# Optimization experiments

Hardware: AMD Instinct MI355X
Metric: run time of the kernel (lower is better)

The kernel has to match this reference:

```python
import jax, jax.numpy as jnp
import numpy as np

N = 100000      # nodes
E = 1600000     # edges (before self loops)
G = 64          # graphs (drones)
H = 4           # heads
C = 64          # hidden_channels (per-head dim, concat=False)
NODE_F = 32
DRONE_F = 16
OUT = 32
L = 2           # num_layers
LN_EPS = 1e-5
NEG_SLOPE = 0.2


def setup_inputs() -> dict:
    key = jax.random.key(0)
    ks = jax.random.split(key, 20)
    gn = lambda k, shape, s=0.1: jax.random.normal(k, shape, jnp.float32) * s
    inp = {}
    inp["x"] = jax.random.normal(ks[0], (N, NODE_F), jnp.float32)
    inp["drone_feat"] = jax.random.normal(ks[1], (G, DRONE_F), jnp.float32)
    inp["edge_index"] = jax.random.randint(ks[2], (2, E), 0, N, jnp.int32)
    inp["batch"] = jnp.sort(jax.random.randint(ks[3], (N,), 0, G, jnp.int32))
    inp["node_W"] = gn(ks[4], (C, NODE_F)); inp["node_b"] = jnp.zeros((C,), jnp.float32)
    inp["drone_W"] = gn(ks[5], (C, DRONE_F)); inp["drone_b"] = jnp.zeros((C,), jnp.float32)
    for l in range(L):
        kk = jax.random.split(ks[6 + l], 3)
        inp[f"convW{l}"] = gn(kk[0], (H * C, C))
        inp[f"att_src{l}"] = gn(kk[1], (H, C))
        inp[f"att_dst{l}"] = gn(kk[2], (H, C))
        inp[f"convb{l}"] = jnp.zeros((C,), jnp.float32)
        inp[f"ln_g{l}"] = jnp.ones((C,), jnp.float32)
        inp[f"ln_b{l}"] = jnp.zeros((C,), jnp.float32)
    inp["out_W"] = gn(ks[10], (OUT, C)); inp["out_b"] = jnp.zeros((OUT,), jnp.float32)
    return inp


def _layer_norm(x, g, b):
    mu = jnp.mean(x, axis=-1, keepdims=True)
    var = jnp.mean((x - mu) ** 2, axis=-1, keepdims=True)
    return (x - mu) * jax.lax.rsqrt(var + LN_EPS) * g + b


def _gat_conv(h, src, dst, W, a_src, a_dst, b):
    # h: [N, C] -> per-head transform [N, H, C]
    xh = (h @ W.T).reshape(N, H, C)
    alpha_s = jnp.sum(xh * a_src[None], axis=-1)  # [N, H]
    alpha_d = jnp.sum(xh * a_dst[None], axis=-1)  # [N, H]
    e = jax.nn.leaky_relu(alpha_s[src] + alpha_d[dst], NEG_SLOPE)  # [E', H]
    m = jax.ops.segment_max(e, dst, num_segments=N)  # segment softmax over dst
    ex = jnp.exp(e - m[dst])
    s = jax.ops.segment_sum(ex, dst, num_segments=N)
    alpha = ex / (s[dst] + 1e-16)                   # [E', H]
    out = jax.ops.segment_sum(xh[src] * alpha[:, :, None], dst, num_segments=N)
    return jnp.mean(out, axis=1) + b                # concat=False -> head mean


def reference(x, edge_index, drone_feat, batch, node_W, node_b, drone_W, drone_b,
              convW0, att_src0, att_dst0, convb0, ln_g0, ln_b0,
              convW1, att_src1, att_dst1, convb1, ln_g1, ln_b1,
              out_W, out_b):
    # add self loops (PyG GATConv default add_self_loops=True)
    loop = jnp.arange(N, dtype=edge_index.dtype)
    src = jnp.concatenate([edge_index[0], loop])
    dst = jnp.concatenate([edge_index[1], loop])
    h = x @ node_W.T + node_b + (drone_feat @ drone_W.T + drone_b)[batch]
    layers = [(convW0, att_src0, att_dst0, convb0, ln_g0, ln_b0),
              (convW1, att_src1, att_dst1, convb1, ln_g1, ln_b1)]
    for (W, a_s, a_d, cb, g, lb) in layers:
        h = h + jax.nn.relu(_layer_norm(_gat_conv(h, src, dst, W, a_s, a_d, cb), g, lb))
    return h @ out_W.T + out_b
```

## Files before the change

### kernel.cpp

```cpp
#include <hip/hip_runtime.h>
#include <hip/hip_fp16.h>
#include <math.h>


#define NEG_SLOPE 0.2f
#define LN_EPS 1e-5f

struct __align__(8) h16x4 { __half x, y, z, w; };

__global__ void k_scatter(const int* __restrict__ edge_index, int* __restrict__ cnt,
                          int* __restrict__ csrB,
                          const float* __restrict__ cW0, const float* __restrict__ cW1,
                          const float* __restrict__ s0, const float* __restrict__ d0,
                          const float* __restrict__ s1, const float* __restrict__ d1,
                          const float* __restrict__ out_W,
                          float* __restrict__ wt0, float* __restrict__ wt1,
                          float* __restrict__ uv, float* __restrict__ owT,
                          int E, int S) {
    if (blockIdx.y == 0 && blockIdx.x < 128) {
        int i = blockIdx.x * 256 + threadIdx.x;
        {
            int j = i & 16383;
            int co = j >> 6, k = j & 63;
            if (i < 16384) wt0[k * 256 + co] = cW0[j];
            else           wt1[k * 256 + co] = cW1[j];
        }
        if (i < 2048) {
            int k = i >> 5, o = i & 31;
            owT[i] = out_W[o * 64 + k];
        }
        if (i < 1024) {
            int l = i >> 9, sd = (i >> 8) & 1, head = (i >> 6) & 3, kk = i & 63;
            const float* W   = l ? cW1 : cW0;
            const float* att = l ? (sd ? d1 : s1) : (sd ? d0 : s0);
            float acc = 0.f;
            for (int c = 0; c < 64; ++c)
                acc += W[(head * 64 + c) * 64 + kk] * att[head * 64 + c];
            uv[i] = acc;
        }
    }
    int lo = blockIdx.y * S, hi = lo + S;
    int i = (blockIdx.x * blockDim.x + threadIdx.x) * 4;
    if (i + 3 < E) {
        int4 sv = *(const int4*)(edge_index + i);
        int4 dv = *(const int4*)(edge_index + E + i);
        int sl;
        if (dv.x >= lo && dv.x < hi) { sl = atomicAdd(cnt + dv.x, 1); if (sl < 63) csrB[((size_t)dv.x << 6) + 1 + sl] = sv.x; }
        if (dv.y >= lo && dv.y < hi) { sl = atomicAdd(cnt + dv.y, 1); if (sl < 63) csrB[((size_t)dv.y << 6) + 1 + sl] = sv.y; }
        if (dv.z >= lo && dv.z < hi) { sl = atomicAdd(cnt + dv.z, 1); if (sl < 63) csrB[((size_t)dv.z << 6) + 1 + sl] = sv.z; }
        if (dv.w >= lo && dv.w < hi) { sl = atomicAdd(cnt + dv.w, 1); if (sl < 63) csrB[((size_t)dv.w << 6) + 1 + sl] = sv.w; }
    } else {
        for (int k = i; k < E; ++k) {
            int d = edge_index[E + k];
            if (d >= lo && d < hi) {
                int sl = atomicAdd(cnt + d, 1);
                if (sl < 63) csrB[((size_t)d << 6) + 1 + sl] = edge_index[k];
            }
        }
    }
}

#define XPAD 68
template <bool FIRST>
__global__ __launch_bounds__(256) void k_xh(
        const float* __restrict__ h, const float* __restrict__ wt,
        const float* __restrict__ uv_l, __half* __restrict__ xh,
        float* __restrict__ as_, float* __restrict__ ad_,
        const float* __restrict__ x, const int* __restrict__ batch,
        const float* __restrict__ node_W, const float* __restrict__ drone_W,
        const float* __restrict__ node_b, const float* __restrict__ drone_b,
        const float* __restrict__ drone_feat, float* __restrict__ h_out, int N) {
    __shared__ float hs[32][XPAD];
    __shared__ float wn[FIRST ? 32 : 1][FIRST ? 65 : 1];
    __shared__ float wd[FIRST ? 16 : 1][FIRST ? 65 : 1];
    __shared__ float bs[FIRST ? 64 : 1];
    __shared__ float xs[FIRST ? 32 : 1][FIRST ? 33 : 1];
    __shared__ float ds[FIRST ? 32 : 1][FIRST ? 17 : 1];
    int t = threadIdx.x;
    int n0 = blockIdx.x * 32;
    if constexpr (FIRST) {
        for (int i = t; i < 2048; i += 256) { int co = i >> 5, k = i & 31; wn[k][co] = node_W[i]; }
        for (int i = t; i < 1024; i += 256) { int co = i >> 4, k = i & 15; wd[k][co] = drone_W[i]; }
        if (t < 64) bs[t] = node_b[t] + drone_b[t];
        for (int i = t; i < 1024; i += 256) {
            int r = i >> 5, c = i & 31;
            int n = n0 + r;
            xs[r][c] = (n < N) ? x[(size_t)n * 32 + c] : 0.f;
        }
        for (int i = t; i < 512; i += 256) {
            int r = i >> 4, c = i & 15;
            int n = n0 + r;
            int g = (n < N) ? batch[n] : 0;
            ds[r][c] = drone_feat[g * 16 + c];
        }
        __syncthreads();
        int co = t & 63, nsub = t >> 6;
        float b = bs[co];
#pragma unroll
        for (int j = 0; j < 8; ++j) {
            int r = nsub * 8 + j;
            float a = b;
#pragma unroll
            for (int k = 0; k < 32; ++k) a = fmaf(xs[r][k], wn[k][co], a);
#pragma unroll
            for (int k = 0; k < 16; ++k) a = fmaf(ds[r][k], wd[k][co], a);
            hs[r][co] = a;
            int n = n0 + r;
            if (n < N) h_out[(size_t)n * 64 + co] = a;
        }
        __syncthreads();
    } else {
        for (int i = t; i < 32 * 64; i += 256) {
            int r = i >> 6, c = i & 63;
            int n = n0 + r;
            hs[r][c] = (n < N) ? h[(size_t)n * 64 + c] : 0.f;
        }
        __syncthreads();
    }
    int co4 = (t & 63) * 4;
    int nsub = t >> 6;
    float4 acc[8];
#pragma unroll
    for (int j = 0; j < 8; ++j) acc[j] = make_float4(0.f, 0.f, 0.f, 0.f);
    const float* wp = wt + co4;
#pragma unroll 2
    for (int k4 = 0; k4 < 16; ++k4) {
        float4 w0 = *(const float4*)(wp + (k4 * 4 + 0) * 256);
        float4 w1 = *(const float4*)(wp + (k4 * 4 + 1) * 256);
        float4 w2 = *(const float4*)(wp + (k4 * 4 + 2) * 256);
        float4 w3 = *(const float4*)(wp + (k4 * 4 + 3) * 256);
#pragma unroll
        for (int j = 0; j < 8; ++j) {
            float4 hv = *(const float4*)&hs[nsub * 8 + j][k4 * 4];
            float4 a = acc[j];
            a.x = fmaf(hv.x, w0.x, fmaf(hv.y, w1.x, fmaf(hv.z, w2.x, fmaf(hv.w, w3.x, a.x))));
            a.y = fmaf(hv.x, w0.y, fmaf(hv.y, w1.y, fmaf(hv.z, w2.y, fmaf(hv.w, w3.y, a.y))));
            a.z = fmaf(hv.x, w0.z, fmaf(hv.y, w1.z, fmaf(hv.z, w2.z, fmaf(hv.w, w3.z, a.z))));
            a.w = fmaf(hv.x, w0.w, fmaf(hv.y, w1.w, fmaf(hv.z, w2.w, fmaf(hv.w, w3.w, a.w))));
            acc[j] = a;
        }
    }
#pragma unroll
    for (int j = 0; j < 8; ++j) {
        int n = n0 + nsub * 8 + j;
        if (n < N) {
            h16x4 o;
            o.x = __float2half(acc[j].x);
            o.y = __float2half(acc[j].y);
            o.z = __float2half(acc[j].z);
            o.w = __float2half(acc[j].w);
            *(h16x4*)(xh + (size_t)n * 256 + co4) = o;
        }
    }
    {
        int row  = t >> 3;
        int head = (t >> 1) & 3;
        int sd   = t & 1;
        int n = n0 + row;
        if (n < N) {
            const float* u = uv_l + sd * 256 + head * 64;
            float a = 0.f;
#pragma unroll
            for (int k4 = 0; k4 < 16; ++k4) {
                float4 hv = *(const float4*)&hs[row][k4 * 4];
                float4 uu = *(const float4*)(u + k4 * 4);
                a += hv.x * uu.x + hv.y * uu.y + hv.z * uu.z + hv.w * uu.w;
            }
            (sd ? ad_ : as_)[n * 4 + head] = a;
        }
    }
}

__device__ __forceinline__ __half2 shxor_h2(__half2 a, int m) {
    int u = __shfl_xor(*(int*)&a, m, 64);
    return *(__half2*)&u;
}

template <bool LAST>
__global__ __launch_bounds__(256) void k_gat(
        const __half* __restrict__ xh, const float* __restrict__ as_,
        const float* __restrict__ ad_, const int* __restrict__ cnt,
        const int* __restrict__ csrB, const float* __restrict__ convb,
        const float* __restrict__ ln_g, const float* __restrict__ ln_b,
        float* __restrict__ h, const float* __restrict__ owT,
        const float* __restrict__ out_b, float* __restrict__ out, int N) {
    __shared__ float owT_lds[2048];
    __shared__ float hout_lds4[4][64];
    int t = threadIdx.x;
    int wid = t >> 6, lane = t & 63;
    if (LAST) {
        for (int i = t; i < 2048; i += 256) owT_lds[i] = owT[i];
        __syncthreads();
    }
    int n = blockIdx.x * 4 + wid;
    if (n >= N) return;
    float* hout_lds = hout_lds4[wid];
    int g    = lane >> 4;
    int l16  = lane & 15;
    int head = l16 >> 2;
    int r0 = n << 6;
    int r1 = r0 + 1 + min(cnt[n], 63);
    float adv = ad_[(size_t)n * 4 + head];
    const char* xbb = (const char*)xh + (l16 << 5);
    const char* asb = (const char*)as_ + (head << 2);
    const char* cbb = (const char*)csrB;

    float s = 0.f;
    __half2 acc[8];
#pragma unroll
    for (int j = 0; j < 8; ++j) acc[j] = __float2half2_rn(0.f);

    uint4 zero4 = make_uint4(0u, 0u, 0u, 0u);
    int idx;
    idx = r0 + g;      bool vA = idx < r1; int sA = n; if (g != 0 && vA) sA = *(const int*)(cbb + ((unsigned)idx << 2));
    idx = r0 + 4 + g;  bool vB = idx < r1; int sB = 0; if (vB) sB = *(const int*)(cbb + ((unsigned)idx << 2));
    idx = r0 + 8 + g;  bool vC = idx < r1; int sC = 0; if (vC) sC = *(const int*)(cbb + ((unsigned)idx << 2));
    idx = r0 + 12 + g; bool vD = idx < r1; int sD = 0; if (vD) sD = *(const int*)(cbb + ((unsigned)idx << 2));
    float asA = 0.f, asB = 0.f;
    uint4 qA0 = zero4, qA1 = zero4, qB0 = zero4, qB1 = zero4;
    if (vA) {
        asA = *(const float*)(asb + ((unsigned)sA << 4));
        const uint4* bp = (const uint4*)(xbb + ((unsigned)sA << 9));
        qA0 = bp[0]; qA1 = bp[1];
    }
    if (vB) {
        asB = *(const float*)(asb + ((unsigned)sB << 4));
        const uint4* bp = (const uint4*)(xbb + ((unsigned)sB << 9));
        qB0 = bp[0]; qB1 = bp[1];
    }

    auto COMPUTE = [&](bool vc, float asc, const uint4& q0, const uint4& q1) {
        float e = asc + adv;
        e = e > 0.f ? e : NEG_SLOPE * e;
        float w = __expf(e);
        w = vc ? w : 0.f;
        s += w;
        __half2 w2 = __float2half2_rn(w);
        const __half2* ha = (const __half2*)&q0;
        const __half2* hb = (const __half2*)&q1;
        acc[0] = __hfma2(w2, ha[0], acc[0]);
        acc[1] = __hfma2(w2, ha[1], acc[1]);
        acc[2] = __hfma2(w2, ha[2], acc[2]);
        acc[3] = __hfma2(w2, ha[3], acc[3]);
        acc[4] = __hfma2(w2, hb[0], acc[4]);
        acc[5] = __hfma2(w2, hb[1], acc[5]);
        acc[6] = __hfma2(w2, hb[2], acc[6]);
        acc[7] = __hfma2(w2, hb[3], acc[7]);
    };

    for (int i = r0; i < r1; i += 8) {
        COMPUTE(vA, asA, qA0, qA1);
        int idxE = i + 16 + g; bool vE = idxE < r1; int sE = 0;
        if (vE) sE = *(const int*)(cbb + ((unsigned)idxE << 2));
        vA = vC;
        if (vC) {
            asA = *(const float*)(asb + ((unsigned)sC << 4));
            const uint4* bp = (const uint4*)(xbb + ((unsigned)sC << 9));
            qA0 = bp[0]; qA1 = bp[1];
        }
        COMPUTE(vB, asB, qB0, qB1);
        int idxF = i + 20 + g; bool vF = idxF < r1; int sF = 0;
        if (vF) sF = *(const int*)(cbb + ((unsigned)idxF << 2));
        vB = vD;
        if (vD) {
            asB = *(const float*)(asb + ((unsigned)sD << 4));
            const uint4* bp = (const uint4*)(xbb + ((unsigned)sD << 9));
            qB0 = bp[0]; qB1 = bp[1];
        }
        vC = vE; sC = sE;
        vD = vF; sD = sF;
    }

    s += __shfl_xor(s, 16, 64);
    s += __shfl_xor(s, 32, 64);
#pragma unroll
    for (int j = 0; j < 8; ++j) {
        acc[j] = __hadd2(acc[j], shxor_h2(acc[j], 16));
        acc[j] = __hadd2(acc[j], shxor_h2(acc[j], 32));
    }
    float inv = 1.f / (s + 1e-16f);
    __half2 ih = __float2half2_rn(inv);
#pragma unroll
    for (int j = 0; j < 8; ++j) {
        acc[j] = __hmul2(acc[j], ih);
        acc[j] = __hadd2(acc[j], shxor_h2(acc[j], 4));
        acc[j] = __hadd2(acc[j], shxor_h2(acc[j], 8));
    }
    float f[16];
#pragma unroll
    for (int j = 0; j < 8; ++j) {
        float2 tv = __half22float2(acc[j]);
        f[2 * j]     = tv.x;
        f[2 * j + 1] = tv.y;
    }
    int cblk = lane & 3;
    int cb16 = cblk * 16;
    float o[16];
    float part = 0.f;
#pragma unroll
    for (int q = 0; q < 4; ++q) {
        float4 cb = *(const float4*)(convb + cb16 + q * 4);
        o[q * 4 + 0] = 0.25f * f[q * 4 + 0] + cb.x;
        o[q * 4 + 1] = 0.25f * f[q * 4 + 1] + cb.y;
        o[q * 4 + 2] = 0.25f * f[q * 4 + 2] + cb.z;
        o[q * 4 + 3] = 0.25f * f[q * 4 + 3] + cb.w;
        part += o[q * 4 + 0] + o[q * 4 + 1] + o[q * 4 + 2] + o[q * 4 + 3];
    }
    part += __shfl_xor(part, 1, 64);
    part += __shfl_xor(part, 2, 64);
    float mu = part * (1.f / 64.f);
    float vs = 0.f;
#pragma unroll
    for (int j = 0; j < 16; ++j) { o[j] -= mu; vs += o[j] * o[j]; }
    vs += __shfl_xor(vs, 1, 64);
    vs += __shfl_xor(vs, 2, 64);
    float rstd = rsqrtf(vs * (1.f / 64.f) + LN_EPS);

    if (!LAST) {
        if (lane < 4) {
            float4* hp = (float4*)(h + (size_t)n * 64 + cb16);
#pragma unroll
            for (int q = 0; q < 4; ++q) {
                float4 hv = hp[q];
                float4 gv = *(const float4*)(ln_g + cb16 + q * 4);
                float4 bv = *(const float4*)(ln_b + cb16 + q * 4);
                hv.x += fmaxf(o[q * 4 + 0] * rstd * gv.x + bv.x, 0.f);
                hv.y += fmaxf(o[q * 4 + 1] * rstd * gv.y + bv.y, 0.f);
                hv.z += fmaxf(o[q * 4 + 2] * rstd * gv.z + bv.z, 0.f);
                hv.w += fmaxf(o[q * 4 + 3] * rstd * gv.w + bv.w, 0.f);
                hp[q] = hv;
            }
        }
    } else {
        if (lane < 4) {
            const float4* hp = (const float4*)(h + (size_t)n * 64 + cb16);
#pragma unroll
            for (int q = 0; q < 4; ++q) {
                float4 hv = hp[q];
                float4 gv = *(const float4*)(ln_g + cb16 + q * 4);
                float4 bv = *(const float4*)(ln_b + cb16 + q * 4);
                hout_lds[cb16 + q * 4 + 0] = hv.x + fmaxf(o[q * 4 + 0] * rstd * gv.x + bv.x, 0.f);
                hout_lds[cb16 + q * 4 + 1] = hv.y + fmaxf(o[q * 4 + 1] * rstd * gv.y + bv.y, 0.f);
                hout_lds[cb16 + q * 4 + 2] = hv.z + fmaxf(o[q * 4 + 2] * rstd * gv.z + bv.z, 0.f);
                hout_lds[cb16 + q * 4 + 3] = hv.w + fmaxf(o[q * 4 + 3] * rstd * gv.w + bv.w, 0.f);
            }
        }
        asm volatile("s_waitcnt lgkmcnt(0)" ::: "memory");
        if (lane < 32) {
            float acc2 = out_b[lane];
#pragma unroll 8
            for (int k = 0; k < 64; ++k)
                acc2 = fmaf(hout_lds[k], owT_lds[k * 32 + lane], acc2);
            out[(size_t)n * 32 + lane] = acc2;
        }
    }
}

static inline unsigned cdiv(long long a, long long b) { return (unsigned)((a + b - 1) / b); }

extern "C" void kernel_launch(void* const* d_in, const int* in_sizes, int n_in,
                              void* d_out, int out_size, void* d_ws, size_t ws_size,
                              hipStream_t stream) {
    const float* x          = (const float*)d_in[0];
    const float* drone_feat = (const float*)d_in[1];
    const int*   edge_index = (const int*)d_in[2];
    const int*   batch      = (const int*)d_in[3];
    const float* node_W     = (const float*)d_in[4];
    const float* node_b     = (const float*)d_in[5];
    const float* drone_W    = (const float*)d_in[6];
    const float* drone_b    = (const float*)d_in[7];
    const float* convW[2]   = {(const float*)d_in[8],  (const float*)d_in[14]};
    const float* att_src[2] = {(const float*)d_in[9],  (const float*)d_in[15]};
    const float* att_dst[2] = {(const float*)d_in[10], (const float*)d_in[16]};
    const float* convb[2]   = {(const float*)d_in[11], (const float*)d_in[17]};
    const float* ln_g[2]    = {(const float*)d_in[12], (const float*)d_in[18]};
    const float* ln_b[2]    = {(const float*)d_in[13], (const float*)d_in[19]};
    const float* out_W      = (const float*)d_in[20];
    const float* out_b      = (const float*)d_in[21];
    float* out = (float*)d_out;

    const int N = in_sizes[0] / 32;
    const int E = in_sizes[2] / 2;
    const int P = 8;
    const int S = cdiv(N, P);

    char* base = (char*)d_ws;
    size_t off = 0;
    auto alloc = [&](size_t bytes) {
        char* p = base + off;
        off = (off + bytes + 255) & ~(size_t)255;
        return p;
    };
    float*           h      = (float*)alloc((size_t)N * 64 * 4);
    __half*          xh     = (__half*)alloc((size_t)N * 256 * 2);
    float*           as_    = (float*)alloc((size_t)N * 4 * 4);
    float*           ad_    = (float*)alloc((size_t)N * 4 * 4);
    float*           wt0    = (float*)alloc((size_t)256 * 64 * 4);
    float*           wt1    = (float*)alloc((size_t)256 * 64 * 4);
    float*           uv     = (float*)alloc((size_t)1024 * 4);
    float*           owT    = (float*)alloc((size_t)2048 * 4);
    int*             cnt    = (int*)alloc((size_t)N * 4);
    int*             csrB   = (int*)alloc((size_t)N * 64 * 4);
    (void)ws_size;
    const float* wt[2] = {wt0, wt1};

    (void)hipMemsetAsync(cnt, 0, (size_t)N * 4, stream);
    {
        dim3 g(cdiv(cdiv(E, 4), 256), P);
        k_scatter<<<g, 256, 0, stream>>>(edge_index, cnt, csrB,
                                         convW[0], convW[1], att_src[0], att_dst[0],
                                         att_src[1], att_dst[1], out_W,
                                         wt0, wt1, uv, owT, E, S);
    }
    k_xh<true><<<cdiv(N, 32), 256, 0, stream>>>(h, wt[0], uv + 0 * 512, xh, as_, ad_,
                                                x, batch, node_W, drone_W, node_b,
                                                drone_b, drone_feat, h, N);
    k_gat<false><<<cdiv(N, 4), 256, 0, stream>>>(xh, as_, ad_, cnt, csrB, convb[0],
                                                 ln_g[0], ln_b[0], h, owT, out_b, out, N);
    k_xh<false><<<cdiv(N, 32), 256, 0, stream>>>(h, wt[1], uv + 1 * 512, xh, as_, ad_,
                                                 x, batch, node_W, drone_W, node_b,
                                                 drone_b, drone_feat, h, N);
    k_gat<true><<<cdiv(N, 4), 256, 0, stream>>>(xh, as_, ad_, cnt, csrB, convb[1],
                                                ln_g[1], ln_b[1], h, owT, out_b, out, N);
}
```

Before: 632.2 us.

## Merge edge scatter and first-layer feature transform into one kernel launch

Replaces the memset plus scatter kernel with a small init kernel that zeroes counts and prepares layer-0 weights. The CSR scatter blocks and the layer-0 embedding and xh blocks then run as disjoint block ranges of a single kernel, so the two independent stages can overlap on the GPU. The combined kernel reserves the larger shared-memory footprint for every block, including the scatter blocks, which may lower occupancy for the atomic-heavy part.

```diff
diff --git a/kernel.cpp b/kernel.cpp
--- a/kernel.cpp
+++ b/kernel.cpp
@@ -8,115 +8,196 @@
 
 struct __align__(8) h16x4 { __half x, y, z, w; };
 
-__global__ void k_scatter(const int* __restrict__ edge_index, int* __restrict__ cnt,
-                          int* __restrict__ csrB,
-                          const float* __restrict__ cW0, const float* __restrict__ cW1,
-                          const float* __restrict__ s0, const float* __restrict__ d0,
-                          const float* __restrict__ s1, const float* __restrict__ d1,
-                          const float* __restrict__ out_W,
-                          float* __restrict__ wt0, float* __restrict__ wt1,
-                          float* __restrict__ uv, float* __restrict__ owT,
-                          int E, int S) {
-    if (blockIdx.y == 0 && blockIdx.x < 128) {
-        int i = blockIdx.x * 256 + threadIdx.x;
-        {
-            int j = i & 16383;
-            int co = j >> 6, k = j & 63;
-            if (i < 16384) wt0[k * 256 + co] = cW0[j];
-            else           wt1[k * 256 + co] = cW1[j];
-        }
-        if (i < 2048) {
-            int k = i >> 5, o = i & 31;
-            owT[i] = out_W[o * 64 + k];
-        }
-        if (i < 1024) {
-            int l = i >> 9, sd = (i >> 8) & 1, head = (i >> 6) & 3, kk = i & 63;
-            const float* W   = l ? cW1 : cW0;
-            const float* att = l ? (sd ? d1 : s1) : (sd ? d0 : s0);
-            float acc = 0.f;
-            for (int c = 0; c < 64; ++c)
-                acc += W[(head * 64 + c) * 64 + kk] * att[head * 64 + c];
-            uv[i] = acc;
-        }
-    }
-    int lo = blockIdx.y * S, hi = lo + S;
-    int i = (blockIdx.x * blockDim.x + threadIdx.x) * 4;
-    if (i + 3 < E) {
-        int4 sv = *(const int4*)(edge_index + i);
-        int4 dv = *(const int4*)(edge_index + E + i);
-        int sl;
-        if (dv.x >= lo && dv.x < hi) { sl = atomicAdd(cnt + dv.x, 1); if (sl < 63) csrB[((size_t)dv.x << 6) + 1 + sl] = sv.x; }
-        if (dv.y >= lo && dv.y < hi) { sl = atomicAdd(cnt + dv.y, 1); if (sl < 63) csrB[((size_t)dv.y << 6) + 1 + sl] = sv.y; }
-        if (dv.z >= lo && dv.z < hi) { sl = atomicAdd(cnt + dv.z, 1); if (sl < 63) csrB[((size_t)dv.z << 6) + 1 + sl] = sv.z; }
-        if (dv.w >= lo && dv.w < hi) { sl = atomicAdd(cnt + dv.w, 1); if (sl < 63) csrB[((size_t)dv.w << 6) + 1 + sl] = sv.w; }
-    } else {
-        for (int k = i; k < E; ++k) {
-            int d = edge_index[E + k];
-            if (d >= lo && d < hi) {
-                int sl = atomicAdd(cnt + d, 1);
-                if (sl < 63) csrB[((size_t)d << 6) + 1 + sl] = edge_index[k];
+__global__ __launch_bounds__(256) void k_init(
+        const float* __restrict__ cW0, const float* __restrict__ s0,
+        const float* __restrict__ d0, float* __restrict__ wt0,
+        float* __restrict__ uv, int* __restrict__ cnt, int N) {
+    int i = blockIdx.x * 256 + threadIdx.x;
+    if (i < N) cnt[i] = 0;
+    if (i < 16384) { int co = i >> 6, k = i & 63; wt0[k * 256 + co] = cW0[i]; }
+    if (i < 512) {
+        int sd = (i >> 8) & 1, head = (i >> 6) & 3, kk = i & 63;
+        const float* att = sd ? d0 : s0;
+        float acc = 0.f;
+        for (int c = 0; c < 64; ++c)
+            acc += cW0[(head * 64 + c) * 64 + kk] * att[head * 64 + c];
+        uv[i] = acc;
+    }
+}
+
+#define XPAD 68
+__device__ __forceinline__ void xh0_block(
+        int n0, const float* __restrict__ wt, const float* __restrict__ uv_l,
+        __half* __restrict__ xh, float* __restrict__ as_, float* __restrict__ ad_,
+        const float* __restrict__ x, const int* __restrict__ batch,
+        const float* __restrict__ node_W, const float* __restrict__ drone_W,
+        const float* __restrict__ node_b, const float* __restrict__ drone_b,
+        const float* __restrict__ drone_feat, float* __restrict__ h_out, int N,
+        float (*hs)[XPAD], float (*wn)[65], float (*wd)[65], float* bs,
+        float (*xs)[33], float (*ds)[17]) {
+    int t = threadIdx.x;
+    for (int i = t; i < 2048; i += 256) { int co = i >> 5, k = i & 31; wn[k][co] = node_W[i]; }
+    for (int i = t; i < 1024; i += 256) { int co = i >> 4, k = i & 15; wd[k][co] = drone_W[i]; }
+    if (t < 64) bs[t] = node_b[t] + drone_b[t];
+    for (int i = t; i < 1024; i += 256) {
+        int r = i >> 5, c = i & 31;
+        int n = n0 + r;
+        xs[r][c] = (n < N) ? x[(size_t)n * 32 + c] : 0.f;
+    }
+    for (int i = t; i < 512; i += 256) {
+        int r = i >> 4, c = i & 15;
+        int n = n0 + r;
+        int g = (n < N) ? batch[n] : 0;
+        ds[r][c] = drone_feat[g * 16 + c];
+    }
+    __syncthreads();
+    {
+        int co = t & 63, nsub = t >> 6;
+        float b = bs[co];
+#pragma unroll
+        for (int j = 0; j < 8; ++j) {
+            int r = nsub * 8 + j;
+            float a = b;
+#pragma unroll
+            for (int k = 0; k < 32; ++k) a = fmaf(xs[r][k], wn[k][co], a);
+#pragma unroll
+            for (int k = 0; k < 16; ++k) a = fmaf(ds[r][k], wd[k][co], a);
+            hs[r][co] = a;
+            int n = n0 + r;
+            if (n < N) h_out[(size_t)n * 64 + co] = a;
+        }
+    }
+    __syncthreads();
+    int co4 = (t & 63) * 4;
+    int nsub = t >> 6;
+    float4 acc[8];
+#pragma unroll
+    for (int j = 0; j < 8; ++j) acc[j] = make_float4(0.f, 0.f, 0.f, 0.f);
+    const float* wp = wt + co4;
+#pragma unroll 2
+    for (int k4 = 0; k4 < 16; ++k4) {
+        float4 w0 = *(const float4*)(wp + (k4 * 4 + 0) * 256);
+        float4 w1 = *(const float4*)(wp + (k4 * 4 + 1) * 256);
+        float4 w2 = *(const float4*)(wp + (k4 * 4 + 2) * 256);
+        float4 w3 = *(const float4*)(wp + (k4 * 4 + 3) * 256);
+#pragma unroll
+        for (int j = 0; j < 8; ++j) {
+            float4 hv = *(const float4*)&hs[nsub * 8 + j][k4 * 4];
+            float4 a = acc[j];
+            a.x = fmaf(hv.x, w0.x, fmaf(hv.y, w1.x, fmaf(hv.z, w2.x, fmaf(hv.w, w3.x, a.x))));
+            a.y = fmaf(hv.x, w0.y, fmaf(hv.y, w1.y, fmaf(hv.z, w2.y, fmaf(hv.w, w3.y, a.y))));
+            a.z = fmaf(hv.x, w0.z, fmaf(hv.y, w1.z, fmaf(hv.z, w2.z, fmaf(hv.w, w3.z, a.z))));
+            a.w = fmaf(hv.x, w0.w, fmaf(hv.y, w1.w, fmaf(hv.z, w2.w, fmaf(hv.w, w3.w, a.w))));
+            acc[j] = a;
+        }
+    }
+#pragma unroll
+    for (int j = 0; j < 8; ++j) {
+        int n = n0 + nsub * 8 + j;
+        if (n < N) {
+            h16x4 o;
+            o.x = __float2half(acc[j].x);
+            o.y = __float2half(acc[j].y);
+            o.z = __float2half(acc[j].z);
+            o.w = __float2half(acc[j].w);
+            *(h16x4*)(xh + (size_t)n * 256 + co4) = o;
+        }
+    }
+    {
+        int row  = t >> 3;
+        int head = (t >> 1) & 3;
+        int sd   = t & 1;
+        int n = n0 + row;
+        if (n < N) {
+            const float* u = uv_l + sd * 256 + head * 64;
+            float a = 0.f;
+#pragma unroll
+            for (int k4 = 0; k4 < 16; ++k4) {
+                float4 hv = *(const float4*)&hs[row][k4 * 4];
+                float4 uu = *(const float4*)(u + k4 * 4);
+                a += hv.x * uu.x + hv.y * uu.y + hv.z * uu.z + hv.w * uu.w;
             }
-        }
-    }
-}
-
-#define XPAD 68
-template <bool FIRST>
-__global__ __launch_bounds__(256) void k_xh(
-        const float* __restrict__ h, const float* __restrict__ wt,
-        const float* __restrict__ uv_l, __half* __restrict__ xh,
+            (sd ? ad_ : as_)[n * 4 + head] = a;
+        }
+    }
+}
+
+__global__ __launch_bounds__(256) void k_sx(
+        const int* __restrict__ edge_index, int* __restrict__ cnt,
+        int* __restrict__ csrB,
+        const float* __restrict__ cW1, const float* __restrict__ s1,
+        const float* __restrict__ d1, const float* __restrict__ out_W,
+        float* __restrict__ wt1, float* __restrict__ uv, float* __restrict__ owT,
+        int E, int S, int NS,
+        const float* __restrict__ wt0, __half* __restrict__ xh,
         float* __restrict__ as_, float* __restrict__ ad_,
         const float* __restrict__ x, const int* __restrict__ batch,
         const float* __restrict__ node_W, const float* __restrict__ drone_W,
         const float* __restrict__ node_b, const float* __restrict__ drone_b,
         const float* __restrict__ drone_feat, float* __restrict__ h_out, int N) {
     __shared__ float hs[32][XPAD];
-    __shared__ float wn[FIRST ? 32 : 1][FIRST ? 65 : 1];
-    __shared__ float wd[FIRST ? 16 : 1][FIRST ? 65 : 1];
-    __shared__ float bs[FIRST ? 64 : 1];
-    __shared__ float xs[FIRST ? 32 : 1][FIRST ? 33 : 1];
-    __shared__ float ds[FIRST ? 32 : 1][FIRST ? 17 : 1];
+    __shared__ float wn[32][65];
+    __shared__ float wd[16][65];
+    __shared__ float bs[64];
+    __shared__ float xs[32][33];
+    __shared__ float ds[32][17];
+    int bid = blockIdx.x;
+    int SCAT = NS * 8;
+    if (bid < SCAT) {
+        if (bid < 128) {
+            int i = bid * 256 + threadIdx.x;
+            if (i < 16384) { int co = i >> 6, k = i & 63; wt1[k * 256 + co] = cW1[i]; }
+            if (i < 2048) { int k = i >> 5, o = i & 31; owT[i] = out_W[o * 64 + k]; }
+            if (i < 512) {
+                int sd = (i >> 8) & 1, head = (i >> 6) & 3, kk = i & 63;
+                const float* att = sd ? d1 : s1;
+                float acc = 0.f;
+                for (int c = 0; c < 64; ++c)
+                    acc += cW1[(head * 64 + c) * 64 + kk] * att[head * 64 + c];
+                uv[512 + i] = acc;
+            }
+        }
+        int pass = bid / NS, bx = bid - pass * NS;
+        int lo = pass * S, hi = lo + S;
+        int i = (bx * 256 + threadIdx.x) * 4;
+        if (i + 3 < E) {
+            int4 sv = *(const int4*)(edge_index + i);
+            int4 dv = *(const int4*)(edge_index + E + i);
+            int sl;
+            if (dv.x >= lo && dv.x < hi) { sl = atomicAdd(cnt + dv.x, 1); if (sl < 63) csrB[((size_t)dv.x << 6) + 1 + sl] = sv.x; }
+            if (dv.y >= lo && dv.y < hi) { sl = atomicAdd(cnt + dv.y, 1); if (sl < 63) csrB[((size_t)dv.y << 6) + 1 + sl] = sv.y; }
+            if (dv.z >= lo && dv.z < hi) { sl = atomicAdd(cnt + dv.z, 1); if (sl < 63) csrB[((size_t)dv.z << 6) + 1 + sl] = sv.z; }
+            if (dv.w >= lo && dv.w < hi) { sl = atomicAdd(cnt + dv.w, 1); if (sl < 63) csrB[((size_t)dv.w << 6) + 1 + sl] = sv.w; }
+        } else {
+            for (int k = i; k < E; ++k) {
+                int d = edge_index[E + k];
+                if (d >= lo && d < hi) {
+                    int sl = atomicAdd(cnt + d, 1);
+                    if (sl < 63) csrB[((size_t)d << 6) + 1 + sl] = edge_index[k];
+                }
+            }
+        }
+    } else {
+        int n0 = (bid - SCAT) * 32;
+        xh0_block(n0, wt0, uv, xh, as_, ad_, x, batch, node_W, drone_W,
+                  node_b, drone_b, drone_feat, h_out, N,
+                  hs, wn, wd, bs, xs, ds);
+    }
+}
+
+__global__ __launch_bounds__(256) void k_xh1(
+        const float* __restrict__ h, const float* __restrict__ wt,
+        const float* __restrict__ uv_l, __half* __restrict__ xh,
+        float* __restrict__ as_, float* __restrict__ ad_, int N) {
+    __shared__ float hs[32][XPAD];
     int t = threadIdx.x;
     int n0 = blockIdx.x * 32;
-    if constexpr (FIRST) {
-        for (int i = t; i < 2048; i += 256) { int co = i >> 5, k = i & 31; wn[k][co] = node_W[i]; }
-        for (int i = t; i < 1024; i += 256) { int co = i >> 4, k = i & 15; wd[k][co] = drone_W[i]; }
-        if (t < 64) bs[t] = node_b[t] + drone_b[t];
-        for (int i = t; i < 1024; i += 256) {
-            int r = i >> 5, c = i & 31;
-            int n = n0 + r;
-            xs[r][c] = (n < N) ? x[(size_t)n * 32 + c] : 0.f;
-        }
-        for (int i = t; i < 512; i += 256) {
-            int r = i >> 4, c = i & 15;
-            int n = n0 + r;
-            int g = (n < N) ? batch[n] : 0;
-            ds[r][c] = drone_feat[g * 16 + c];
-        }
-        __syncthreads();
-        int co = t & 63, nsub = t >> 6;
-        float b = bs[co];
-#pragma unroll
-        for (int j = 0; j < 8; ++j) {
-            int r = nsub * 8 + j;
-            float a = b;
-#pragma unroll
-            for (int k = 0; k < 32; ++k) a = fmaf(xs[r][k], wn[k][co], a);
-#pragma unroll
-            for (int k = 0; k < 16; ++k) a = fmaf(ds[r][k], wd[k][co], a);
-            hs[r][co] = a;
-            int n = n0 + r;
-            if (n < N) h_out[(size_t)n * 64 + co] = a;
-        }
-        __syncthreads();
-    } else {
-        for (int i = t; i < 32 * 64; i += 256) {
-            int r = i >> 6, c = i & 63;
-            int n = n0 + r;
-            hs[r][c] = (n < N) ? h[(size_t)n * 64 + c] : 0.f;
-        }
-        __syncthreads();
-    }
+    for (int i = t; i < 32 * 64; i += 256) {
+        int r = i >> 6, c = i & 63;
+        int n = n0 + r;
+        hs[r][c] = (n < N) ? h[(size_t)n * 64 + c] : 0.f;
+    }
+    __syncthreads();
     int co4 = (t & 63) * 4;
     int nsub = t >> 6;
     float4 acc[8];
@@ -383,6 +464,7 @@
     const int E = in_sizes[2] / 2;
     const int P = 8;
     const int S = cdiv(N, P);
+    const int NS = cdiv(cdiv(E, 4), 256);
 
     char* base = (char*)d_ws;
     size_t off = 0;
@@ -402,24 +484,18 @@
     int*             cnt    = (int*)alloc((size_t)N * 4);
     int*             csrB   = (int*)alloc((size_t)N * 64 * 4);
     (void)ws_size;
-    const float* wt[2] = {wt0, wt1};
-
-    (void)hipMemsetAsync(cnt, 0, (size_t)N * 4, stream);
-    {
-        dim3 g(cdiv(cdiv(E, 4), 256), P);
-        k_scatter<<<g, 256, 0, stream>>>(edge_index, cnt, csrB,
-                                         convW[0], convW[1], att_src[0], att_dst[0],
-                                         att_src[1], att_dst[1], out_W,
-                                         wt0, wt1, uv, owT, E, S);
-    }
-    k_xh<true><<<cdiv(N, 32), 256, 0, stream>>>(h, wt[0], uv + 0 * 512, xh, as_, ad_,
-                                                x, batch, node_W, drone_W, node_b,
-                                                drone_b, drone_feat, h, N);
+
+    k_init<<<cdiv(N, 256), 256, 0, stream>>>(convW[0], att_src[0], att_dst[0],
+                                             wt0, uv, cnt, N);
+    k_sx<<<NS * P + cdiv(N, 32), 256, 0, stream>>>(
+        edge_index, cnt, csrB,
+        convW[1], att_src[1], att_dst[1], out_W,
+        wt1, uv, owT, E, S, NS,
+        wt0, xh, as_, ad_,
+        x, batch, node_W, drone_W, node_b, drone_b, drone_feat, h, N);
     k_gat<false><<<cdiv(N, 4), 256, 0, stream>>>(xh, as_, ad_, cnt, csrB, convb[0],
                                                  ln_g[0], ln_b[0], h, owT, out_b, out, N);
-    k_xh<false><<<cdiv(N, 32), 256, 0, stream>>>(h, wt[1], uv + 1 * 512, xh, as_, ad_,
-                                                 x, batch, node_W, drone_W, node_b,
-                                                 drone_b, drone_feat, h, N);
+    k_xh1<<<cdiv(N, 32), 256, 0, stream>>>(h, wt1, uv + 512, xh, as_, ad_, N);
     k_gat<true><<<cdiv(N, 4), 256, 0, stream>>>(xh, as_, ad_, cnt, csrB, convb[1],
                                                 ln_g[1], ln_b[1], h, owT, out_b, out, N);
 }
```

Result: no change. 622.1 us (-1.6%).
